# Optimization experiments

Measured on AMD Instinct MI355X. Metric: run time of the kernel, lower is better.

Reference implementation:

```python
import jax, jax.numpy as jnp
import numpy as np


def _cdist_l2(a, b):
    # a: [b,k,D], b: [b,k,D] -> [b,k,k], matches torch.cdist(p=2)
    a2 = jnp.sum(a * a, axis=-1)[:, :, None]
    b2 = jnp.sum(b * b, axis=-1)[:, None, :]
    ab = jnp.einsum('bkd,bjd->bkj', a, b)
    return jnp.sqrt(jnp.maximum(a2 + b2 - 2.0 * ab, 0.0))


def _solve_lsa(cost):
    """Exact Hungarian (Jonker-Volgenant shortest augmenting path, O(n^3))
    on a square cost matrix [n,n]. Returns col_of_row: assigned column per row,
    identical to scipy.optimize.linear_sum_assignment's second return (first is arange).
    1-indexed arrays with a dummy slot 0, classic e-maxx formulation."""
    n = cost.shape[0]
    INF = jnp.float32(1e30)

    def row_body(i, carry):
        u, v, p = carry  # u,v: potentials [n+1]; p[j] = row matched to col j
        way = jnp.zeros(n + 1, jnp.int32)
        minv = jnp.full(n + 1, INF, jnp.float32)
        used = jnp.zeros(n + 1, bool)
        p = p.at[0].set(jnp.int32(i))

        def cond(c):
            j0, p, u, v, way, minv, used = c
            return p[j0] != 0

        def body(c):
            j0, p, u, v, way, minv, used = c
            used = used.at[j0].set(True)
            i0 = p[j0]
            cur = cost[i0 - 1, :] - u[i0] - v[1:]          # reduced costs, cols 1..n
            free = ~used[1:]
            better = free & (cur < minv[1:])
            minv = minv.at[1:].set(jnp.where(better, cur, minv[1:]))
            way = way.at[1:].set(jnp.where(better, j0, way[1:]))
            cand = jnp.where(free, minv[1:], INF)
            jmin = jnp.argmin(cand)
            delta = cand[jmin]
            j1 = (jmin + 1).astype(jnp.int32)
            u = u.at[p].add(jnp.where(used, delta, 0.0))   # u[p[j]] += delta for used j
            v = jnp.where(used, v - delta, v)
            minv = jnp.where(used, minv, minv - delta)
            return (j1, p, u, v, way, minv, used)

        j0 = jnp.int32(0)
        j0, p, u, v, way, minv, used = jax.lax.while_loop(
            cond, body, (j0, p, u, v, way, minv, used))

        # augment along alternating path
        def aug_cond(c):
            j0, p = c
            return j0 != 0

        def aug(c):
            j0, p = c
            j1 = way[j0]
            return (j1, p.at[j0].set(p[j1]))

        _, p = jax.lax.while_loop(aug_cond, aug, (j0, p))
        return (u, v, p)

    u0 = jnp.zeros(n + 1, jnp.float32)
    v0 = jnp.zeros(n + 1, jnp.float32)
    p0 = jnp.zeros(n + 1, jnp.int32)
    _, _, p = jax.lax.fori_loop(1, n + 1, row_body, (u0, v0, p0))
    # p[j] = row of col j  ->  invert to col of row
    col_of_row = jnp.zeros(n, jnp.int32).at[p[1:] - 1].set(jnp.arange(n, dtype=jnp.int32))
    return col_of_row


def setup_inputs() -> dict:
    key = jax.random.key(0)
    k1, k2 = jax.random.split(key)
    B, K, D = 16, 64, 50176  # b, k group masks, h*w = 224*224
    outputs = jax.random.normal(k1, (B, K, D), dtype=jnp.float32)
    targets = jax.random.normal(k2, (B, K, D), dtype=jnp.float32)
    return {"outputs": outputs, "targets": targets}


def reference(outputs, targets):
    # cost_type == 'L2'
    cost_mask = _cdist_l2(outputs, targets)                 # [b,k,k]
    inds2 = jax.vmap(_solve_lsa)(cost_mask)                 # [b,k] matched target idx per pred
    b, k = inds2.shape
    inds = jnp.broadcast_to(jnp.arange(k, dtype=jnp.int32), (b, k))  # scipy row_ind is arange
    return (inds, inds2)
```

## Files before the change

kernel.cpp:

```cpp
#include <hip/hip_runtime.h>

#define DD 50176
#define NB 16
#define NK 64

constexpr int KSPLIT = 64;
constexpr int KTILE  = 49;
constexpr int TKK    = 16;

__global__ __launch_bounds__(256) void gemm_partial(const float* __restrict__ A,
                                                    const float* __restrict__ B,
                                                    float* __restrict__ ws) {
  const int b = blockIdx.y;
  const int w = threadIdx.x >> 6;
  const int lane = threadIdx.x & 63;
  const int s = blockIdx.x * 4 + w;
  const float* Ab = A + (size_t)b * NK * DD;
  const float* Bb = B + (size_t)b * NK * DD;

  __shared__ __align__(16) float lds[4][2][TKK * 64];
  float* As = lds[w][0];
  float* Bs = lds[w][1];

  const int ti = lane >> 3;
  const int tj = lane & 7;
  const int kq = lane & 3;
  const int rr = lane >> 2;

  float c[8][8];
#pragma unroll
  for (int r = 0; r < 8; ++r)
#pragma unroll
    for (int q = 0; q < 8; ++q) c[r][q] = 0.f;
  float a2p[4] = {0.f, 0.f, 0.f, 0.f};
  float b2p[4] = {0.f, 0.f, 0.f, 0.f};
  float4 avr[4], bvr[4];

  const int kbase = s * (KTILE * TKK);
#pragma unroll
  for (int f = 0; f < 4; ++f) {
    const int row = f * 16 + rr;
    avr[f] = *reinterpret_cast<const float4*>(Ab + (size_t)row * DD + kbase + kq * 4);
    bvr[f] = *reinterpret_cast<const float4*>(Bb + (size_t)row * DD + kbase + kq * 4);
  }

  for (int t = 0; t < KTILE; ++t) {
#pragma unroll
    for (int f = 0; f < 4; ++f) {
      const int row = f * 16 + rr;
      const int col = (row + 8 * kq) & 63;
      const float4 av = avr[f], bv = bvr[f];
      As[(kq * 4 + 0) * 64 + col] = av.x;
      As[(kq * 4 + 1) * 64 + col] = av.y;
      As[(kq * 4 + 2) * 64 + col] = av.z;
      As[(kq * 4 + 3) * 64 + col] = av.w;
      Bs[(kq * 4 + 0) * 64 + col] = bv.x;
      Bs[(kq * 4 + 1) * 64 + col] = bv.y;
      Bs[(kq * 4 + 2) * 64 + col] = bv.z;
      Bs[(kq * 4 + 3) * 64 + col] = bv.w;
      a2p[f] = fmaf(av.x, av.x, a2p[f]); a2p[f] = fmaf(av.y, av.y, a2p[f]);
      a2p[f] = fmaf(av.z, av.z, a2p[f]); a2p[f] = fmaf(av.w, av.w, a2p[f]);
      b2p[f] = fmaf(bv.x, bv.x, b2p[f]); b2p[f] = fmaf(bv.y, bv.y, b2p[f]);
      b2p[f] = fmaf(bv.z, bv.z, b2p[f]); b2p[f] = fmaf(bv.w, bv.w, b2p[f]);
    }
    if (t + 1 < KTILE) {
      const int k0 = kbase + (t + 1) * TKK;
#pragma unroll
      for (int f = 0; f < 4; ++f) {
        const int row = f * 16 + rr;
        avr[f] = *reinterpret_cast<const float4*>(Ab + (size_t)row * DD + k0 + kq * 4);
        bvr[f] = *reinterpret_cast<const float4*>(Bb + (size_t)row * DD + k0 + kq * 4);
      }
    }
#pragma unroll 4
    for (int kk = 0; kk < TKK; ++kk) {
      const int g = 8 * (kk >> 2);
      const float4 a0 = *reinterpret_cast<const float4*>(&As[kk * 64 + ((8 * ti + g) & 63)]);
      const float4 a1 = *reinterpret_cast<const float4*>(&As[kk * 64 + ((8 * ti + 4 + g) & 63)]);
      const float4 b0 = *reinterpret_cast<const float4*>(&Bs[kk * 64 + ((8 * tj + g) & 63)]);
      const float4 b1 = *reinterpret_cast<const float4*>(&Bs[kk * 64 + ((8 * tj + 4 + g) & 63)]);
      const float ar[8] = {a0.x, a0.y, a0.z, a0.w, a1.x, a1.y, a1.z, a1.w};
      const float br[8] = {b0.x, b0.y, b0.z, b0.w, b1.x, b1.y, b1.z, b1.w};
#pragma unroll
      for (int r = 0; r < 8; ++r)
#pragma unroll
        for (int q = 0; q < 8; ++q)
          c[r][q] = fmaf(ar[r], br[q], c[r][q]);
    }
  }

  float* Pab = ws + (size_t)(b * KSPLIT + s) * 4096;
#pragma unroll
  for (int r = 0; r < 8; ++r) {
    *reinterpret_cast<float4*>(Pab + (8 * ti + r) * 64 + 8 * tj) =
        make_float4(c[r][0], c[r][1], c[r][2], c[r][3]);
    *reinterpret_cast<float4*>(Pab + (8 * ti + r) * 64 + 8 * tj + 4) =
        make_float4(c[r][4], c[r][5], c[r][6], c[r][7]);
  }

#pragma unroll
  for (int f = 0; f < 4; ++f) {
    a2p[f] += __shfl_xor(a2p[f], 1, 64);
    a2p[f] += __shfl_xor(a2p[f], 2, 64);
    b2p[f] += __shfl_xor(b2p[f], 1, 64);
    b2p[f] += __shfl_xor(b2p[f], 2, 64);
  }
  if (kq == 0) {
    float* Pa2 = ws + (size_t)NB * KSPLIT * 4096 + (size_t)(b * KSPLIT + s) * 64;
    float* Pb2 = Pa2 + (size_t)NB * KSPLIT * 64;
#pragma unroll
    for (int f = 0; f < 4; ++f) {
      Pa2[f * 16 + rr] = a2p[f];
      Pb2[f * 16 + rr] = b2p[f];
    }
  }
}

template <int NSPLIT>
__global__ __launch_bounds__(256) void reduce_cost(const float* __restrict__ ws,
                                                   float* __restrict__ costg) {
  const int slice = blockIdx.x;
  const int b = blockIdx.y;
  const int tid = threadIdx.x;
  __shared__ double a2s[4], b2s[64];
  const size_t pa2 = (size_t)NB * NSPLIT * 4096;
  const size_t pb2 = pa2 + (size_t)NB * NSPLIT * 64;

  if (tid < 64) {
    double s = 0.0;
    for (int sp = 0; sp < NSPLIT; ++sp)
      s += (double)ws[pb2 + (size_t)(b * NSPLIT + sp) * 64 + tid];
    b2s[tid] = s;
  } else if (tid < 68) {
    const int r = slice * 4 + (tid - 64);
    double s = 0.0;
    for (int sp = 0; sp < NSPLIT; ++sp)
      s += (double)ws[pa2 + (size_t)(b * NSPLIT + sp) * 64 + r];
    a2s[tid - 64] = s;
  }

  const int elem = slice * 256 + tid;
  double acc = 0.0;
  for (int sp = 0; sp < NSPLIT; ++sp)
    acc += (double)ws[(size_t)(b * NSPLIT + sp) * 4096 + elem];
  __syncthreads();

  const int ii = tid >> 6;
  const int j = tid & 63;
  const double c2 = a2s[ii] + b2s[j] - 2.0 * acc;
  costg[(size_t)b * 4096 + elem] = (float)sqrt(c2 > 0.0 ? c2 : 0.0);
}

__device__ __forceinline__ float readlane_f(float x, int lane) {
  return __int_as_float(__builtin_amdgcn_readlane(__float_as_int(x), lane));
}

template <int CTRL, int RMASK>
__device__ __forceinline__ float dpp_mov_inf(float k) {
  return __int_as_float(__builtin_amdgcn_update_dpp(
      0x7F800000, __float_as_int(k), CTRL, RMASK, 0xf, false));
}

template <int CTRL, int RMASK>
__device__ __forceinline__ float dpp_minf_step(float k) {
  return fminf(dpp_mov_inf<CTRL, RMASK>(k), k);
}
__device__ __forceinline__ float dpp_minf(float k) {
  k = dpp_minf_step<0x111, 0xf>(k);
  k = dpp_minf_step<0x112, 0xf>(k);
  k = dpp_minf_step<0x114, 0xf>(k);
  k = dpp_minf_step<0x118, 0xf>(k);
  k = dpp_minf_step<0x142, 0xa>(k);
  k = dpp_minf_step<0x143, 0xc>(k);
  return readlane_f(k, 63);
}

template <int CTRL, int RMASK>
__device__ __forceinline__ void dpp_min2_step(float& m1, float& m2) {
  const float o1 = dpp_mov_inf<CTRL, RMASK>(m1);
  const float o2 = dpp_mov_inf<CTRL, RMASK>(m2);
  const float lo = fminf(m1, o1);
  const float hi = fmaxf(m1, o1);
  m2 = fminf(fminf(m2, o2), hi);
  m1 = lo;
}
__device__ __forceinline__ float2 dpp_min2f(float x) {
  float m1 = x, m2 = __int_as_float(0x7F800000);
  dpp_min2_step<0x111, 0xf>(m1, m2);
  dpp_min2_step<0x112, 0xf>(m1, m2);
  dpp_min2_step<0x114, 0xf>(m1, m2);
  dpp_min2_step<0x118, 0xf>(m1, m2);
  dpp_min2_step<0x142, 0xa>(m1, m2);
  dpp_min2_step<0x143, 0xc>(m1, m2);
  return make_float2(readlane_f(m1, 63), readlane_f(m2, 63));
}

__global__ __launch_bounds__(64) void lsa_solve(const float* __restrict__ costg,
                                                int* __restrict__ out) {
  const int b = blockIdx.x;
  __shared__ float costd[64 * 64];
  const int tid = threadIdx.x;

  for (int e = tid; e < 4096; e += 64)
    costd[e] = costg[(size_t)b * 4096 + e];
  __syncthreads();

  const int l = tid;
  const float INFF = 1e30f;

  float cmin = costd[l];
  int cargmin = 0;
#pragma unroll 8
  for (int r = 1; r < 64; ++r) {
    const float cv = costd[r * 64 + l];
    if (cv < cmin) { cmin = cv; cargmin = r; }
  }
  float v_l = cmin;
  float u_l = 0.0f;
  int p_l = 0;
  int colof_l = 0;
  unsigned long long rowused = 0ULL;
  for (int j = 0; j < 64; ++j) {
    const int rj = __builtin_amdgcn_readlane(cargmin, j);
    if (!((rowused >> rj) & 1ULL)) {
      rowused |= 1ULL << rj;
      if (l == j) p_l = rj + 1;
      if (l == rj) colof_l = j + 1;
    }
  }
  unsigned long long freemask = ~rowused;

  {
    unsigned long long rm = rowused;
    while (rm) {
      const int ri = __ffsll(rm) - 1;
      rm &= rm - 1;
      const int j1 = __builtin_amdgcn_readlane(colof_l, ri) - 1;
      const float red = (l == j1) ? INFF : (costd[ri * 64 + l] - v_l);
      const float rmin = dpp_minf(red);
      if (l == ri) u_l = rmin;
      if (l == j1) v_l -= rmin;
    }
  }

  for (int pass = 0; pass < 2; ++pass) {
    unsigned long long m = freemask;
    while (m) {
      int ir = __ffsll(m);
      m &= m - 1;
      for (int chain = 0; chain < 8; ++chain) {
        if (!((freemask >> (ir - 1)) & 1ULL)) break;
        const float uir = readlane_f(u_l, ir - 1);
        const float curx = costd[(ir - 1) * 64 + l] - uir - v_l;
        const float2 mm = dpp_min2f(curx);
        const float u1 = mm.x;
        const float u2 = mm.y;
        const int j1 = __ffsll(__ballot(curx == u1)) - 1;
        if (l == ir - 1) u_l = uir + u2;
        const bool strict = (u1 < u2);
        if (strict && l == j1) v_l -= (u2 - u1);
        const int k = __builtin_amdgcn_readlane(p_l, j1);
        if (strict || k == 0) {
          if (l == j1) p_l = ir;
          if (l == ir - 1) colof_l = j1 + 1;
          freemask &= ~(1ULL << (ir - 1));
          if (k != 0) {
            if (l == k - 1) colof_l = 0;
            freemask |= 1ULL << (k - 1);
            if (strict) { ir = k; continue; }
          }
          break;
        } else {
          break;
        }
      }
    }
  }

  for (int i_row = 1; i_row <= 64; ++i_row) {
    if (!((freemask >> (i_row - 1)) & 1ULL)) continue;
    float minv = INFF;
    int way_l = 0;
    bool used = false;
    int j0 = 0;
    const bool irow_hit = (l + 1 == i_row);

    while (true) {
      const int i0 = (j0 == 0) ? i_row : __builtin_amdgcn_readlane(p_l, j0 - 1);
      if (i0 == 0) break;
      if (j0 > 0 && l == j0 - 1) used = true;
      const unsigned long long um = __ballot(used);
      const bool addu = irow_hit ||
                        (colof_l != 0 && ((um >> (colof_l - 1)) & 1ULL));
      const float ui0 = readlane_f(u_l, i0 - 1);
      const float cur = costd[(i0 - 1) * 64 + l] - ui0 - v_l;
      if (!used && cur < minv) { minv = cur; way_l = j0; }
      const float cand = used ? INFF : minv;

      const float delta = dpp_minf(cand);
      const int jmin = __ffsll(__ballot(cand == delta)) - 1;

      if (used) v_l -= delta; else minv -= delta;
      if (addu) u_l += delta;
      j0 = jmin + 1;
    }

    while (j0 != 0) {
      const int j1 = __builtin_amdgcn_readlane(way_l, j0 - 1);
      const int pj1 = (j1 == 0) ? i_row : __builtin_amdgcn_readlane(p_l, j1 - 1);
      if (l == j0 - 1) p_l = pj1;
      if (l == pj1 - 1) colof_l = j0;
      j0 = j1;
    }
  }

  out[b * NK + l] = l;
  out[NB * NK + b * NK + l] = colof_l - 1;
}

extern "C" void kernel_launch(void* const* d_in, const int* in_sizes, int n_in,
                              void* d_out, int out_size, void* d_ws, size_t ws_size,
                              hipStream_t stream) {
  const float* A = (const float*)d_in[0];
  const float* B = (const float*)d_in[1];
  float* ws = (float*)d_ws;
  int* out = (int*)d_out;

  const size_t fpart = (size_t)NB * KSPLIT * 4224;
  float* costg = ws + fpart;

  gemm_partial<<<dim3(16, NB), 256, 0, stream>>>(A, B, ws);
  reduce_cost<KSPLIT><<<dim3(16, NB), 256, 0, stream>>>(ws, costg);
  lsa_solve<<<NB, 64, 0, stream>>>(costg, out);
}
```

Baseline: 252.8 us.

## Compute partial Gram matrices with split-bf16 MFMA instead of FP32 FMA

Replaces the scalar FP32 outer-product GEMM with bf16 MFMA 16x16x32 instructions, splitting each float into hi and lo bf16 parts and summing three products to approximate FP32 accuracy. Blocks shrink to two waves each and the grid doubles so the same 64 K-splits are covered. The intent is to move the dominant dot-product work onto matrix cores. The cost is extra conversion ALU work and some loss of precision, which could flip near-tied Hungarian assignments.

```diff
diff --git a/kernel.cpp b/kernel.cpp
--- a/kernel.cpp
+++ b/kernel.cpp
@@ -5,38 +5,54 @@
 #define NK 64
 
 constexpr int KSPLIT = 64;
-constexpr int KTILE  = 49;
-constexpr int TKK    = 16;
-
-__global__ __launch_bounds__(256) void gemm_partial(const float* __restrict__ A,
+constexpr int KPS    = DD / KSPLIT;
+constexpr int NSUB   = 49;
+constexpr int NCHUNK = 25;
+constexpr int RS     = 40;
+
+using f32x4  = __attribute__((ext_vector_type(4))) float;
+using bf16x8 = __attribute__((ext_vector_type(8))) short;
+
+__device__ __forceinline__ ushort f2bf(float x) {
+  unsigned u = __float_as_uint(x);
+  u += 0x7FFFu + ((u >> 16) & 1u);
+  return (ushort)(u >> 16);
+}
+__device__ __forceinline__ float bf2f(ushort h) {
+  return __uint_as_float((unsigned)h << 16);
+}
+
+__global__ __launch_bounds__(128) void gemm_partial(const float* __restrict__ A,
                                                     const float* __restrict__ B,
                                                     float* __restrict__ ws) {
   const int b = blockIdx.y;
   const int w = threadIdx.x >> 6;
   const int lane = threadIdx.x & 63;
-  const int s = blockIdx.x * 4 + w;
+  const int s = blockIdx.x * 2 + w;
   const float* Ab = A + (size_t)b * NK * DD;
   const float* Bb = B + (size_t)b * NK * DD;
 
-  __shared__ __align__(16) float lds[4][2][TKK * 64];
-  float* As = lds[w][0];
-  float* Bs = lds[w][1];
-
-  const int ti = lane >> 3;
-  const int tj = lane & 7;
+  __shared__ short smem[2][2][2][64 * RS];
+  short* Ahi = smem[w][0][0];
+  short* Alo = smem[w][0][1];
+  short* Bhi = smem[w][1][0];
+  short* Blo = smem[w][1][1];
+
   const int kq = lane & 3;
   const int rr = lane >> 2;
-
-  float c[8][8];
-#pragma unroll
-  for (int r = 0; r < 8; ++r)
-#pragma unroll
-    for (int q = 0; q < 8; ++q) c[r][q] = 0.f;
+  const int lrow = lane & 15;
+  const int koff = (lane >> 4) * 8;
+
+  f32x4 acc[4][4];
+#pragma unroll
+  for (int m = 0; m < 4; ++m)
+#pragma unroll
+    for (int n = 0; n < 4; ++n) acc[m][n] = f32x4{0.f, 0.f, 0.f, 0.f};
   float a2p[4] = {0.f, 0.f, 0.f, 0.f};
   float b2p[4] = {0.f, 0.f, 0.f, 0.f};
   float4 avr[4], bvr[4];
 
-  const int kbase = s * (KTILE * TKK);
+  const int kbase = s * KPS;
 #pragma unroll
   for (int f = 0; f < 4; ++f) {
     const int row = f * 16 + rr;
@@ -44,59 +60,83 @@
     bvr[f] = *reinterpret_cast<const float4*>(Bb + (size_t)row * DD + kbase + kq * 4);
   }
 
-  for (int t = 0; t < KTILE; ++t) {
-#pragma unroll
-    for (int f = 0; f < 4; ++f) {
-      const int row = f * 16 + rr;
-      const int col = (row + 8 * kq) & 63;
-      const float4 av = avr[f], bv = bvr[f];
-      As[(kq * 4 + 0) * 64 + col] = av.x;
-      As[(kq * 4 + 1) * 64 + col] = av.y;
-      As[(kq * 4 + 2) * 64 + col] = av.z;
-      As[(kq * 4 + 3) * 64 + col] = av.w;
-      Bs[(kq * 4 + 0) * 64 + col] = bv.x;
-      Bs[(kq * 4 + 1) * 64 + col] = bv.y;
-      Bs[(kq * 4 + 2) * 64 + col] = bv.z;
-      Bs[(kq * 4 + 3) * 64 + col] = bv.w;
-      a2p[f] = fmaf(av.x, av.x, a2p[f]); a2p[f] = fmaf(av.y, av.y, a2p[f]);
-      a2p[f] = fmaf(av.z, av.z, a2p[f]); a2p[f] = fmaf(av.w, av.w, a2p[f]);
-      b2p[f] = fmaf(bv.x, bv.x, b2p[f]); b2p[f] = fmaf(bv.y, bv.y, b2p[f]);
-      b2p[f] = fmaf(bv.z, bv.z, b2p[f]); b2p[f] = fmaf(bv.w, bv.w, b2p[f]);
-    }
-    if (t + 1 < KTILE) {
-      const int k0 = kbase + (t + 1) * TKK;
+  for (int c = 0; c < NCHUNK; ++c) {
+    const int halves = (c < NCHUNK - 1) ? 2 : 1;
+    for (int h = 0; h < halves; ++h) {
 #pragma unroll
       for (int f = 0; f < 4; ++f) {
         const int row = f * 16 + rr;
-        avr[f] = *reinterpret_cast<const float4*>(Ab + (size_t)row * DD + k0 + kq * 4);
-        bvr[f] = *reinterpret_cast<const float4*>(Bb + (size_t)row * DD + k0 + kq * 4);
-      }
-    }
-#pragma unroll 4
-    for (int kk = 0; kk < TKK; ++kk) {
-      const int g = 8 * (kk >> 2);
-      const float4 a0 = *reinterpret_cast<const float4*>(&As[kk * 64 + ((8 * ti + g) & 63)]);
-      const float4 a1 = *reinterpret_cast<const float4*>(&As[kk * 64 + ((8 * ti + 4 + g) & 63)]);
-      const float4 b0 = *reinterpret_cast<const float4*>(&Bs[kk * 64 + ((8 * tj + g) & 63)]);
-      const float4 b1 = *reinterpret_cast<const float4*>(&Bs[kk * 64 + ((8 * tj + 4 + g) & 63)]);
-      const float ar[8] = {a0.x, a0.y, a0.z, a0.w, a1.x, a1.y, a1.z, a1.w};
-      const float br[8] = {b0.x, b0.y, b0.z, b0.w, b1.x, b1.y, b1.z, b1.w};
-#pragma unroll
-      for (int r = 0; r < 8; ++r)
-#pragma unroll
-        for (int q = 0; q < 8; ++q)
-          c[r][q] = fmaf(ar[r], br[q], c[r][q]);
+        const int base = row * RS + h * 16 + kq * 4;
+        const float4 av = avr[f], bv = bvr[f];
+        const ushort ah0 = f2bf(av.x), ah1 = f2bf(av.y), ah2 = f2bf(av.z), ah3 = f2bf(av.w);
+        const ushort al0 = f2bf(av.x - bf2f(ah0)), al1 = f2bf(av.y - bf2f(ah1));
+        const ushort al2 = f2bf(av.z - bf2f(ah2)), al3 = f2bf(av.w - bf2f(ah3));
+        const ushort bh0 = f2bf(bv.x), bh1 = f2bf(bv.y), bh2 = f2bf(bv.z), bh3 = f2bf(bv.w);
+        const ushort bl0 = f2bf(bv.x - bf2f(bh0)), bl1 = f2bf(bv.y - bf2f(bh1));
+        const ushort bl2 = f2bf(bv.z - bf2f(bh2)), bl3 = f2bf(bv.w - bf2f(bh3));
+        *reinterpret_cast<short4*>(&Ahi[base]) = make_short4(ah0, ah1, ah2, ah3);
+        *reinterpret_cast<short4*>(&Alo[base]) = make_short4(al0, al1, al2, al3);
+        *reinterpret_cast<short4*>(&Bhi[base]) = make_short4(bh0, bh1, bh2, bh3);
+        *reinterpret_cast<short4*>(&Blo[base]) = make_short4(bl0, bl1, bl2, bl3);
+        a2p[f] = fmaf(av.x, av.x, a2p[f]); a2p[f] = fmaf(av.y, av.y, a2p[f]);
+        a2p[f] = fmaf(av.z, av.z, a2p[f]); a2p[f] = fmaf(av.w, av.w, a2p[f]);
+        b2p[f] = fmaf(bv.x, bv.x, b2p[f]); b2p[f] = fmaf(bv.y, bv.y, b2p[f]);
+        b2p[f] = fmaf(bv.z, bv.z, b2p[f]); b2p[f] = fmaf(bv.w, bv.w, b2p[f]);
+      }
+      const int st = 2 * c + h + 1;
+      if (st < NSUB) {
+        const int k0 = kbase + st * 16;
+#pragma unroll
+        for (int f = 0; f < 4; ++f) {
+          const int row = f * 16 + rr;
+          avr[f] = *reinterpret_cast<const float4*>(Ab + (size_t)row * DD + k0 + kq * 4);
+          bvr[f] = *reinterpret_cast<const float4*>(Bb + (size_t)row * DD + k0 + kq * 4);
+        }
+      }
+    }
+    if (c == NCHUNK - 1) {
+      const short4 z4 = make_short4(0, 0, 0, 0);
+#pragma unroll
+      for (int f = 0; f < 4; ++f) {
+        const int base = (f * 16 + rr) * RS + 16 + kq * 4;
+        *reinterpret_cast<short4*>(&Ahi[base]) = z4;
+        *reinterpret_cast<short4*>(&Alo[base]) = z4;
+        *reinterpret_cast<short4*>(&Bhi[base]) = z4;
+        *reinterpret_cast<short4*>(&Blo[base]) = z4;
+      }
+    }
+    bf16x8 bhf[4], blf[4];
+#pragma unroll
+    for (int n = 0; n < 4; ++n) {
+      const int r = 16 * n + lrow;
+      bhf[n] = *reinterpret_cast<const bf16x8*>(&Bhi[r * RS + koff]);
+      blf[n] = *reinterpret_cast<const bf16x8*>(&Blo[r * RS + koff]);
+    }
+#pragma unroll
+    for (int m = 0; m < 4; ++m) {
+      const int r = 16 * m + lrow;
+      const bf16x8 ahf = *reinterpret_cast<const bf16x8*>(&Ahi[r * RS + koff]);
+      const bf16x8 alf = *reinterpret_cast<const bf16x8*>(&Alo[r * RS + koff]);
+#pragma unroll
+      for (int n = 0; n < 4; ++n) {
+        acc[m][n] = __builtin_amdgcn_mfma_f32_16x16x32_bf16(ahf, bhf[n], acc[m][n], 0, 0, 0);
+        acc[m][n] = __builtin_amdgcn_mfma_f32_16x16x32_bf16(ahf, blf[n], acc[m][n], 0, 0, 0);
+        acc[m][n] = __builtin_amdgcn_mfma_f32_16x16x32_bf16(alf, bhf[n], acc[m][n], 0, 0, 0);
+      }
     }
   }
 
   float* Pab = ws + (size_t)(b * KSPLIT + s) * 4096;
-#pragma unroll
-  for (int r = 0; r < 8; ++r) {
-    *reinterpret_cast<float4*>(Pab + (8 * ti + r) * 64 + 8 * tj) =
-        make_float4(c[r][0], c[r][1], c[r][2], c[r][3]);
-    *reinterpret_cast<float4*>(Pab + (8 * ti + r) * 64 + 8 * tj + 4) =
-        make_float4(c[r][4], c[r][5], c[r][6], c[r][7]);
-  }
+  const int drow0 = (lane >> 4) * 4;
+#pragma unroll
+  for (int m = 0; m < 4; ++m)
+#pragma unroll
+    for (int n = 0; n < 4; ++n) {
+      const int col = 16 * n + lrow;
+#pragma unroll
+      for (int r = 0; r < 4; ++r)
+        Pab[(16 * m + drow0 + r) * 64 + col] = acc[m][n][r];
+    }
 
 #pragma unroll
   for (int f = 0; f < 4; ++f) {
@@ -329,7 +369,7 @@
   const size_t fpart = (size_t)NB * KSPLIT * 4224;
   float* costg = ws + fpart;
 
-  gemm_partial<<<dim3(16, NB), 256, 0, stream>>>(A, B, ws);
+  gemm_partial<<<dim3(KSPLIT / 2, NB), 128, 0, stream>>>(A, B, ws);
   reduce_cost<KSPLIT><<<dim3(16, NB), 256, 0, stream>>>(ws, costg);
   lsa_solve<<<NB, 64, 0, stream>>>(costg, out);
 }
```

Result: no change. 256.1 us (+1.3%).
